# Kernel tuning notes

Hardware: AMD Instinct MI355X
Metric: run time of the kernel (lower is better)

## Reference

```python
import jax, jax.numpy as jnp
import numpy as np

N_NODES = 50000
N_EDGES = 800000
IN_F = 256
OUT_F = 64


def setup_inputs() -> dict:
    key = jax.random.key(0)
    k1, k2, k3, k4, k5 = jax.random.split(key, 5)
    x = jax.random.normal(k1, (N_NODES, IN_F), dtype=jnp.float32)
    # xavier-uniform-like init for weight
    limit = float(np.sqrt(6.0 / (IN_F + OUT_F)))
    weight = jax.random.uniform(k2, (IN_F, OUT_F), dtype=jnp.float32, minval=-limit, maxval=limit)
    bias = jnp.zeros((1, OUT_F), dtype=jnp.float32)
    edge_weight = jax.random.uniform(k3, (N_EDGES,), dtype=jnp.float32)
    edge_src = jax.random.randint(k4, (N_EDGES,), 0, N_NODES, dtype=jnp.int32)
    edge_dst = jax.random.randint(k5, (N_EDGES,), 0, N_NODES, dtype=jnp.int32)
    return {"x": x, "weight": weight, "bias": bias,
            "edge_weight": edge_weight, "edge_src": edge_src, "edge_dst": edge_dst}


def reference(x, weight, bias, edge_weight, edge_src, edge_dst):
    # in_features (256) > out_features (64): transform first, then propagate.
    h = x @ weight                                  # [N, out]
    # spmm with COO adjacency: out[dst] += w_e * h[src]
    msgs = h[edge_src] * edge_weight[:, None]       # [E, out]
    out = jax.ops.segment_sum(msgs, edge_dst, num_segments=x.shape[0])  # [N, out]
    return out + bias
```

## Files before the change

kernel.cpp:

```cpp
#include <hip/hip_runtime.h>
#include <hip/hip_bf16.h>

#define N_NODES 50000
#define N_EDGES 800000
#define IN_F 256
#define OUT_F 64

#define CAP 64
#define NBKT 16
#define BKT_CAP 51200

typedef __attribute__((ext_vector_type(8))) short short8;
typedef __attribute__((ext_vector_type(4))) float f32x4;

static __device__ __forceinline__ ushort f2bf(float v) {
    __hip_bfloat16 b = __float2bfloat16(v);
    return *(ushort*)&b;
}
static __device__ __forceinline__ int bkt_of(int dst) {
    return (int)(((unsigned long long)(unsigned)dst * 1374390ull) >> 32);
}

__global__ __launch_bounds__(256) void gc_prep(const float* __restrict__ W,
                                               ushort* __restrict__ Wb,
                                               int* __restrict__ cnt,
                                               int* __restrict__ cursor) {
    const int g = blockIdx.x * 256 + threadIdx.x;
    if (g < N_NODES) cnt[g] = 0;
    if (g < NBKT) cursor[g] = 0;
    if (g < 2048) {
        const int s = g >> 9;
        const int kk = (g >> 6) & 7;
        const int lane = g & 63;
        const int n = s * 16 + (lane & 15);
        const int kb = kk * 32 + (lane >> 4) * 8;
#pragma unroll
        for (int j = 0; j < 8; ++j)
            Wb[(size_t)g * 8 + j] = f2bf(W[(kb + j) * OUT_F + n]);
    }
}

__global__ __launch_bounds__(256) void gc_bucket(const int* __restrict__ esrc,
                                                 const int* __restrict__ edst,
                                                 const float* __restrict__ ew,
                                                 int* __restrict__ cursor,
                                                 uint2* __restrict__ arena) {
    __shared__ int hist[NBKT];
    __shared__ int base[NBKT];
    const int t = threadIdx.x;
    if (t < NBKT) hist[t] = 0;
    __syncthreads();

    const int e = blockIdx.x * 1024 + t * 4;
    const bool valid = e < N_EDGES;
    int b[4], loff[4];
    uint2 ent[4];
    if (valid) {
        const int4 s4 = *(const int4*)(esrc + e);
        const int4 d4 = *(const int4*)(edst + e);
        const float4 w4 = *(const float4*)(ew + e);
        const int ds[4] = {d4.x, d4.y, d4.z, d4.w};
        const int ss[4] = {s4.x, s4.y, s4.z, s4.w};
        const float wf[4] = {w4.x, w4.y, w4.z, w4.w};
#pragma unroll
        for (int j = 0; j < 4; ++j) {
            b[j] = bkt_of(ds[j]);
            ent[j].x = (unsigned)ds[j];
            ent[j].y = ((unsigned)f2bf(wf[j]) << 16) | (unsigned)(ss[j] & 0xFFFF);
            loff[j] = atomicAdd(&hist[b[j]], 1);
        }
    }
    __syncthreads();
    if (t < NBKT) base[t] = atomicAdd(&cursor[t], hist[t]);
    __syncthreads();
    if (valid) {
#pragma unroll
        for (int j = 0; j < 4; ++j)
            arena[(size_t)b[j] * BKT_CAP + base[b[j]] + loff[j]] = ent[j];
    }
}

__global__ __launch_bounds__(256) void gc_place2(const uint2* __restrict__ arena,
                                                 const int* __restrict__ cursor,
                                                 int* __restrict__ cnt,
                                                 unsigned int* __restrict__ slots) {
    const int b = blockIdx.x & (NBKT - 1);
    const int j = blockIdx.x >> 4;
    const int n = cursor[b];
    const int i = j * 1024 + threadIdx.x * 4;
    if (i >= n) return;

    const uint2* __restrict__ p = arena + (size_t)b * BKT_CAP + i;
    const uint4 e01 = *(const uint4*)p;
    const uint4 e23 = *(const uint4*)(p + 2);

    const unsigned dd[4] = {e01.x, e01.z, e23.x, e23.z};
    const unsigned sw[4] = {e01.y, e01.w, e23.y, e23.w};
#pragma unroll
    for (int k = 0; k < 4; ++k) {
        if (i + k < n) {
            const int pos = atomicAdd(&cnt[dd[k]], 1);
            if (pos < CAP) slots[(size_t)dd[k] * CAP + pos] = sw[k];
        }
    }
}

__global__ __launch_bounds__(256) void gc_gemm(const float* __restrict__ x,
                                               const ushort* __restrict__ Wb,
                                               ushort* __restrict__ h) {
    __shared__ ushort xs[32 * 264];
    const int t = threadIdx.x;
    const int nbase = blockIdx.x * 32;

    {
#pragma unroll
        for (int i = 0; i < 8; ++i) {
            const int idx = t + i * 256;
            const int node = idx >> 6;
            const int c4 = idx & 63;
            int gnode = nbase + node;
            if (gnode >= N_NODES) gnode = N_NODES - 1;
            const float4 v = ((const float4*)x)[(size_t)gnode * 64 + c4];
            ushort4 bv;
            bv.x = f2bf(v.x); bv.y = f2bf(v.y); bv.z = f2bf(v.z); bv.w = f2bf(v.w);
            *(ushort4*)&xs[node * 264 + c4 * 4] = bv;
        }
    }

    const int s = t >> 6;
    const int lane = t & 63;
    const int m = lane & 15;
    const int quad = lane >> 4;

    short8 bfrag[8];
#pragma unroll
    for (int kk = 0; kk < 8; ++kk)
        bfrag[kk] = *(const short8*)(Wb + ((size_t)(s * 8 + kk) * 64 + lane) * 8);

    __syncthreads();

    f32x4 acc0 = {0.f, 0.f, 0.f, 0.f};
    f32x4 acc1 = {0.f, 0.f, 0.f, 0.f};
#pragma unroll
    for (int kk = 0; kk < 8; ++kk) {
        const short8 a0 = *(const short8*)&xs[m * 264 + kk * 32 + quad * 8];
        const short8 a1 = *(const short8*)&xs[(16 + m) * 264 + kk * 32 + quad * 8];
        acc0 = __builtin_amdgcn_mfma_f32_16x16x32_bf16(a0, bfrag[kk], acc0, 0, 0, 0);
        acc1 = __builtin_amdgcn_mfma_f32_16x16x32_bf16(a1, bfrag[kk], acc1, 0, 0, 0);
    }

#pragma unroll
    for (int r = 0; r < 4; ++r) {
        const int row0 = nbase + quad * 4 + r;
        const int row1 = row0 + 16;
        if (row0 < N_NODES) h[(size_t)row0 * OUT_F + s * 16 + m] = f2bf(acc0[r]);
        if (row1 < N_NODES) h[(size_t)row1 * OUT_F + s * 16 + m] = f2bf(acc1[r]);
    }
}

__global__ __launch_bounds__(256) void gc_gather(const ushort* __restrict__ h,
                                                 const unsigned int* __restrict__ slots,
                                                 const int* __restrict__ cnt,
                                                 const float* __restrict__ bias,
                                                 float* __restrict__ out) {
    const int wid = __builtin_amdgcn_readfirstlane(
        (int)((blockIdx.x * 256 + threadIdx.x) >> 6));
    const int f = threadIdx.x & 63;
    const int d0 = wid * 8;
    if (d0 >= N_NODES) return;

    const int4 ca = *(const int4*)(cnt + d0);
    const int4 cb = *(const int4*)(cnt + d0 + 4);
    const int dg0 = min(ca.x, CAP), dg1 = min(ca.y, CAP);
    const int dg2 = min(ca.z, CAP), dg3 = min(ca.w, CAP);
    const int dg4 = min(cb.x, CAP), dg5 = min(cb.y, CAP);
    const int dg6 = min(cb.z, CAP), dg7 = min(cb.w, CAP);
    const int mdeg = max(max(max(dg0, dg1), max(dg2, dg3)),
                         max(max(dg4, dg5), max(dg6, dg7)));

    const unsigned sw0 = (f < dg0) ? slots[(size_t)(d0 + 0) * CAP + f] : 0u;
    const unsigned sw1 = (f < dg1) ? slots[(size_t)(d0 + 1) * CAP + f] : 0u;
    const unsigned sw2 = (f < dg2) ? slots[(size_t)(d0 + 2) * CAP + f] : 0u;
    const unsigned sw3 = (f < dg3) ? slots[(size_t)(d0 + 3) * CAP + f] : 0u;
    const unsigned sw4 = (f < dg4) ? slots[(size_t)(d0 + 4) * CAP + f] : 0u;
    const unsigned sw5 = (f < dg5) ? slots[(size_t)(d0 + 5) * CAP + f] : 0u;
    const unsigned sw6 = (f < dg6) ? slots[(size_t)(d0 + 6) * CAP + f] : 0u;
    const unsigned sw7 = (f < dg7) ? slots[(size_t)(d0 + 7) * CAP + f] : 0u;

    const float b = bias[f];
    float a0 = b, a1 = b, a2 = b, a3 = b, a4 = b, a5 = b, a6 = b, a7 = b;

    const ushort* __restrict__ hf = h + f;

#define ROWLD(sw, l) \
    hf[(size_t)((unsigned)__builtin_amdgcn_readlane((int)(sw), (l)) & 0xFFFFu) * OUT_F]
#define WBITS(sw, l) \
    __uint_as_float((unsigned)__builtin_amdgcn_readlane((int)(sw), (l)) & 0xFFFF0000u)

    for (int i0 = 0; i0 < mdeg; i0 += 8) {
        unsigned hv0[8], hv1[8], hv2[8], hv3[8], hv4[8], hv5[8], hv6[8], hv7[8];
#pragma unroll
        for (int j = 0; j < 8; ++j) {
            const int l = i0 + j;
            hv0[j] = ROWLD(sw0, l);
            hv1[j] = ROWLD(sw1, l);
            hv2[j] = ROWLD(sw2, l);
            hv3[j] = ROWLD(sw3, l);
            hv4[j] = ROWLD(sw4, l);
            hv5[j] = ROWLD(sw5, l);
            hv6[j] = ROWLD(sw6, l);
            hv7[j] = ROWLD(sw7, l);
        }
#pragma unroll
        for (int j = 0; j < 8; ++j) {
            const int l = i0 + j;
            a0 += WBITS(sw0, l) * __uint_as_float(hv0[j] << 16);
            a1 += WBITS(sw1, l) * __uint_as_float(hv1[j] << 16);
            a2 += WBITS(sw2, l) * __uint_as_float(hv2[j] << 16);
            a3 += WBITS(sw3, l) * __uint_as_float(hv3[j] << 16);
            a4 += WBITS(sw4, l) * __uint_as_float(hv4[j] << 16);
            a5 += WBITS(sw5, l) * __uint_as_float(hv5[j] << 16);
            a6 += WBITS(sw6, l) * __uint_as_float(hv6[j] << 16);
            a7 += WBITS(sw7, l) * __uint_as_float(hv7[j] << 16);
        }
    }
#undef ROWLD
#undef WBITS

    out[(size_t)(d0 + 0) * OUT_F + f] = a0;
    out[(size_t)(d0 + 1) * OUT_F + f] = a1;
    out[(size_t)(d0 + 2) * OUT_F + f] = a2;
    out[(size_t)(d0 + 3) * OUT_F + f] = a3;
    out[(size_t)(d0 + 4) * OUT_F + f] = a4;
    out[(size_t)(d0 + 5) * OUT_F + f] = a5;
    out[(size_t)(d0 + 6) * OUT_F + f] = a6;
    out[(size_t)(d0 + 7) * OUT_F + f] = a7;
}

extern "C" void kernel_launch(void* const* d_in, const int* in_sizes, int n_in,
                              void* d_out, int out_size, void* d_ws, size_t ws_size,
                              hipStream_t stream) {
    const float* x    = (const float*)d_in[0];
    const float* W    = (const float*)d_in[1];
    const float* bias = (const float*)d_in[2];
    const float* ew   = (const float*)d_in[3];
    const int* src    = (const int*)d_in[4];
    const int* dst    = (const int*)d_in[5];
    float* out = (float*)d_out;

    char* ws = (char*)d_ws;
    uint2* arena        = (uint2*)ws;
    ushort* h           = (ushort*)ws;
    int* cnt            = (int*)(ws + 6553600);
    unsigned int* slots = (unsigned int*)(ws + 6753600);
    ushort* Wb          = (ushort*)(ws + 19553600);
    int* cursor         = (int*)(ws + 19586368);

    gc_prep<<<196, 256, 0, stream>>>(W, Wb, cnt, cursor);
    gc_bucket<<<782, 256, 0, stream>>>(src, dst, ew, cursor, arena);
    gc_place2<<<1024, 256, 0, stream>>>(arena, cursor, cnt, slots);
    gc_gemm<<<1563, 256, 0, stream>>>(x, Wb, h);
    gc_gather<<<1563, 256, 0, stream>>>(h, slots, cnt, bias, out);
}
```

Before: 168.7 us.

## Use finer dst buckets with per-block LDS counters in placement

Splits edges into 128 contiguous destination buckets of 391 nodes each instead of 16, so one block can own a whole bucket. The placement kernel then counts slots with LDS atomics and writes cnt once per node. This removes the global atomics on cnt and the separate cnt zeroing in prep. The bucket kernel now handles 8 edges per thread and skips global atomics for empty histogram bins. The trade-off is that placement runs on only 128 blocks, each a serial loop over about 6250 edges, which gives low parallelism. The BKT_CAP of 6912 also truncates any bucket that overflows, which risks dropping edges.

Result: faster. 144.1 us (-14.5%).

```diff
diff --git a/kernel.cpp b/kernel.cpp
--- a/kernel.cpp
+++ b/kernel.cpp
@@ -7,8 +7,9 @@
 #define OUT_F 64
 
 #define CAP 64
-#define NBKT 16
-#define BKT_CAP 51200
+#define NBKT 128
+#define DST_PER_BKT 391
+#define BKT_CAP 6912
 
 typedef __attribute__((ext_vector_type(8))) short short8;
 typedef __attribute__((ext_vector_type(4))) float f32x4;
@@ -17,18 +18,13 @@
     __hip_bfloat16 b = __float2bfloat16(v);
     return *(ushort*)&b;
 }
-static __device__ __forceinline__ int bkt_of(int dst) {
-    return (int)(((unsigned long long)(unsigned)dst * 1374390ull) >> 32);
-}
 
 __global__ __launch_bounds__(256) void gc_prep(const float* __restrict__ W,
                                                ushort* __restrict__ Wb,
-                                               int* __restrict__ cnt,
                                                int* __restrict__ cursor) {
     const int g = blockIdx.x * 256 + threadIdx.x;
-    if (g < N_NODES) cnt[g] = 0;
     if (g < NBKT) cursor[g] = 0;
-    if (g < 2048) {
+    {
         const int s = g >> 9;
         const int kk = (g >> 6) & 7;
         const int lane = g & 63;
@@ -51,57 +47,65 @@
     if (t < NBKT) hist[t] = 0;
     __syncthreads();
 
-    const int e = blockIdx.x * 1024 + t * 4;
-    const bool valid = e < N_EDGES;
-    int b[4], loff[4];
-    uint2 ent[4];
+    const int e0 = blockIdx.x * 2048 + t * 8;
+    const bool valid = e0 < N_EDGES;
+    int b[8], loff[8];
+    uint2 ent[8];
     if (valid) {
-        const int4 s4 = *(const int4*)(esrc + e);
-        const int4 d4 = *(const int4*)(edst + e);
-        const float4 w4 = *(const float4*)(ew + e);
-        const int ds[4] = {d4.x, d4.y, d4.z, d4.w};
-        const int ss[4] = {s4.x, s4.y, s4.z, s4.w};
-        const float wf[4] = {w4.x, w4.y, w4.z, w4.w};
-#pragma unroll
-        for (int j = 0; j < 4; ++j) {
-            b[j] = bkt_of(ds[j]);
+        const int4 sa = *(const int4*)(esrc + e0);
+        const int4 sb = *(const int4*)(esrc + e0 + 4);
+        const int4 da = *(const int4*)(edst + e0);
+        const int4 db = *(const int4*)(edst + e0 + 4);
+        const float4 wa = *(const float4*)(ew + e0);
+        const float4 wb = *(const float4*)(ew + e0 + 4);
+        const int ds[8] = {da.x, da.y, da.z, da.w, db.x, db.y, db.z, db.w};
+        const int ss[8] = {sa.x, sa.y, sa.z, sa.w, sb.x, sb.y, sb.z, sb.w};
+        const float wf[8] = {wa.x, wa.y, wa.z, wa.w, wb.x, wb.y, wb.z, wb.w};
+#pragma unroll
+        for (int j = 0; j < 8; ++j) {
+            b[j] = ds[j] / DST_PER_BKT;
             ent[j].x = (unsigned)ds[j];
             ent[j].y = ((unsigned)f2bf(wf[j]) << 16) | (unsigned)(ss[j] & 0xFFFF);
             loff[j] = atomicAdd(&hist[b[j]], 1);
         }
     }
     __syncthreads();
-    if (t < NBKT) base[t] = atomicAdd(&cursor[t], hist[t]);
+    if (t < NBKT) {
+        const int hc = hist[t];
+        base[t] = hc ? atomicAdd(&cursor[t], hc) : 0;
+    }
     __syncthreads();
     if (valid) {
 #pragma unroll
-        for (int j = 0; j < 4; ++j)
+        for (int j = 0; j < 8; ++j)
             arena[(size_t)b[j] * BKT_CAP + base[b[j]] + loff[j]] = ent[j];
     }
 }
 
-__global__ __launch_bounds__(256) void gc_place2(const uint2* __restrict__ arena,
+__global__ __launch_bounds__(512) void gc_place2(const uint2* __restrict__ arena,
                                                  const int* __restrict__ cursor,
                                                  int* __restrict__ cnt,
                                                  unsigned int* __restrict__ slots) {
-    const int b = blockIdx.x & (NBKT - 1);
-    const int j = blockIdx.x >> 4;
-    const int n = cursor[b];
-    const int i = j * 1024 + threadIdx.x * 4;
-    if (i >= n) return;
-
-    const uint2* __restrict__ p = arena + (size_t)b * BKT_CAP + i;
-    const uint4 e01 = *(const uint4*)p;
-    const uint4 e23 = *(const uint4*)(p + 2);
-
-    const unsigned dd[4] = {e01.x, e01.z, e23.x, e23.z};
-    const unsigned sw[4] = {e01.y, e01.w, e23.y, e23.w};
-#pragma unroll
-    for (int k = 0; k < 4; ++k) {
-        if (i + k < n) {
-            const int pos = atomicAdd(&cnt[dd[k]], 1);
-            if (pos < CAP) slots[(size_t)dd[k] * CAP + pos] = sw[k];
-        }
+    __shared__ int lcnt[DST_PER_BKT];
+    const int b = blockIdx.x;
+    const int t = threadIdx.x;
+    const int dbase = b * DST_PER_BKT;
+
+    for (int i = t; i < DST_PER_BKT; i += 512) lcnt[i] = 0;
+    __syncthreads();
+
+    const int n = min(cursor[b], BKT_CAP);
+    const uint2* __restrict__ p = arena + (size_t)b * BKT_CAP;
+    for (int i = t; i < n; i += 512) {
+        const uint2 ent = p[i];
+        const int pos = atomicAdd(&lcnt[ent.x - dbase], 1);
+        if (pos < CAP) slots[(size_t)ent.x * CAP + pos] = ent.y;
+    }
+    __syncthreads();
+
+    for (int i = t; i < DST_PER_BKT; i += 512) {
+        const int d = dbase + i;
+        if (d < N_NODES) cnt[d] = lcnt[i];
     }
 }
 
@@ -249,16 +253,16 @@
     float* out = (float*)d_out;
 
     char* ws = (char*)d_ws;
-    uint2* arena        = (uint2*)ws;
     ushort* h           = (ushort*)ws;
-    int* cnt            = (int*)(ws + 6553600);
-    unsigned int* slots = (unsigned int*)(ws + 6753600);
-    ushort* Wb          = (ushort*)(ws + 19553600);
-    int* cursor         = (int*)(ws + 19586368);
-
-    gc_prep<<<196, 256, 0, stream>>>(W, Wb, cnt, cursor);
-    gc_bucket<<<782, 256, 0, stream>>>(src, dst, ew, cursor, arena);
-    gc_place2<<<1024, 256, 0, stream>>>(arena, cursor, cnt, slots);
+    int* cnt            = (int*)(ws + 6400000);
+    unsigned int* slots = (unsigned int*)(ws + 6600000);
+    ushort* Wb          = (ushort*)(ws + 19400000);
+    int* cursor         = (int*)(ws + 19432768);
+    uint2* arena        = (uint2*)(ws + 19433280);
+
+    gc_prep<<<8, 256, 0, stream>>>(W, Wb, cursor);
+    gc_bucket<<<391, 256, 0, stream>>>(src, dst, ew, cursor, arena);
+    gc_place2<<<NBKT, 512, 0, stream>>>(arena, cursor, cnt, slots);
     gc_gemm<<<1563, 256, 0, stream>>>(x, Wb, h);
     gc_gather<<<1563, 256, 0, stream>>>(h, slots, cnt, bias, out);
 }
```
